# Performance work log

Measured on AMD Instinct MI355X. Metric: run time of the kernel, lower is better.

Reference implementation:

```python
import jax, jax.numpy as jnp
import numpy as np

EPS = 1e-05
KERNEL_SIZE = 9
KERNEL_VOL = float(KERNEL_SIZE ** 3)

_DN = ("NDHWC", "DHWIO", "NDHWC")


def _box_sum(x, k=KERNEL_SIZE):
    """Sliding-window sum over a k^3 box with SAME zero padding.

    The TF module uses a dense all-ones (k,k,k) conv3d; an all-ones kernel is
    separable, so three 1D passes compute the identical result with O(k) work.
    x: (B, D1, D2, D3, 1) float.
    """
    for kshape in ((k, 1, 1), (1, k, 1), (1, 1, k)):
        w = jnp.ones(kshape + (1, 1), dtype=x.dtype)
        x = jax.lax.conv_general_dilated(
            x, w, window_strides=(1, 1, 1), padding="SAME",
            dimension_numbers=_DN)
    return x


def setup_inputs() -> dict:
    key = jax.random.key(0)
    k1, k2 = jax.random.split(key)
    shape = (2, 192, 192, 192)
    y_true = jax.random.uniform(k1, shape, dtype=jnp.float32)
    y_pred = jax.random.uniform(k2, shape, dtype=jnp.float32)
    return {"y_true": y_true, "y_pred": y_pred}


def reference(y_true, y_pred):
    # Expand (B, D1, D2, D3) -> (B, D1, D2, D3, 1) as in the TF call().
    if y_true.ndim == 4:
        y_true = y_true[..., None]
        y_pred = y_pred[..., None]

    t_sum = _box_sum(y_true)
    p_sum = _box_sum(y_pred)
    tp_sum = _box_sum(y_true * y_pred)

    t_avg = t_sum / KERNEL_VOL
    p_avg = p_sum / KERNEL_VOL

    cross = tp_sum - p_avg * t_sum
    num = cross * cross + EPS  # the DEBUG1 variant returns `num` directly
    return num
```

## Files before the change

### kernel.cpp

```cpp
#include <hip/hip_runtime.h>


#define N 192
#define RSTRIDE 46

#define LDS_BARRIER() asm volatile("s_waitcnt lgkmcnt(0)\n\ts_barrier" ::: "memory")

__global__ __launch_bounds__(1024, 4)
void lncc_kernel(const float* __restrict__ t_in,
                 const float* __restrict__ p_in,
                 float* __restrict__ out)
{
    __shared__ __align__(16) float rowT[3 * 32 * RSTRIDE];
    __shared__ float pcol[3 * 32 * 32];

    const int bid = blockIdx.x;
    int xy, Z, z0;
    if (bid < 64) {
        xy = bid >> 3;
        Z  = 24;
        z0 = (bid & 7) * 24;
    } else {
        const int q  = bid - 64;
        xy = 8 + q / 7;
        const int zi = q % 7;
        if (zi < 3) { Z = 28; z0 = zi * 28; }
        else        { Z = 27; z0 = 84 + (zi - 3) * 27; }
    }
    const int b  = xy / 36;
    const int t6 = xy % 36;
    const int y0 = (t6 / 6) * 32, x0 = (t6 % 6) * 32;
    const int tid = threadIdx.x;

    const int  lf   = tid / 320;
    const int  ls   = tid - lf * 320;
    const int  lry  = ls >> 3;
    const int  lxq  = ls & 7;
    const int  lgy  = y0 - 4 + lry;
    const int  lgx0 = x0 - 4 + 4 * lxq;
    const bool lactive = (tid < 960);
    const bool lyok = ((unsigned)lgy < (unsigned)N);

    const int  cf  = tid >> 8;
    const int  cyq = (tid >> 5) & 7;
    const int  cx  = tid & 31;
    const bool cactive = (tid < 768);

    const int gx = tid & 31;
    const int gy = tid >> 5;

    const size_t plane = (size_t)N * N;
    const float* tb = t_in + (size_t)b * N * plane;
    const float* pb = p_in + (size_t)b * N * plane;
    float*       ob = out  + (size_t)b * N * plane
                           + (size_t)(y0 + gy) * N + (x0 + gx);

    const int lgyc = lyok ? lgy : 0;
    const float* const trow = tb + (size_t)lgyc * N;
    const float* const prow = pb + (size_t)lgyc * N;
    const float* const arow = (lf == 1) ? prow : trow;

    float ring_t[9], ring_p[9], ring_tp[9];
    float sum_t = 0.f, sum_p = 0.f, sum_tp = 0.f;
    #pragma unroll
    for (int i = 0; i < 9; ++i) { ring_t[i] = 0.f; ring_p[i] = 0.f; ring_tp[i] = 0.f; }

    const float4 z4 = make_float4(0.f, 0.f, 0.f, 0.f);

    {
        const int zp0 = z0 - 4;
        float4 fa0 = z4, fa1 = z4, fa2 = z4, fc0 = z4, fc1 = z4, fc2 = z4;
        if (((unsigned)zp0 < (unsigned)N) && lactive && lyok) {
            const float* ar = arow + (size_t)zp0 * plane;
            const float* cr = prow + (size_t)zp0 * plane;
            const int g0 = lgx0, g1 = lgx0 + 4, g2 = lgx0 + 8;
            if ((unsigned)g0 < (unsigned)N) {
                fa0 = *(const float4*)(ar + g0);
                if (lf == 2) fc0 = *(const float4*)(cr + g0);
            }
            if ((unsigned)g1 < (unsigned)N) {
                fa1 = *(const float4*)(ar + g1);
                if (lf == 2) fc1 = *(const float4*)(cr + g1);
            }
            if ((unsigned)g2 < (unsigned)N) {
                fa2 = *(const float4*)(ar + g2);
                if (lf == 2) fc2 = *(const float4*)(cr + g2);
            }
        }
        if (lactive) {
            float4 A0 = fa0, A1 = fa1, A2 = fa2;
            if (lf == 2) {
                A0.x *= fc0.x; A0.y *= fc0.y; A0.z *= fc0.z; A0.w *= fc0.w;
                A1.x *= fc1.x; A1.y *= fc1.y; A1.z *= fc1.z; A1.w *= fc1.w;
                A2.x *= fc2.x; A2.y *= fc2.y; A2.z *= fc2.z; A2.w *= fc2.w;
            }
            const float v0 = A0.x, v1 = A0.y, v2  = A0.z, v3  = A0.w;
            const float v4 = A1.x, v5 = A1.y, v6  = A1.z, v7  = A1.w;
            const float v8 = A2.x, v9 = A2.y, v10 = A2.z, v11 = A2.w;
            float s0 = ((v0+v1) + (v2+v3)) + ((v4+v5) + (v6+v7)) + v8;
            float s1 = s0 - v0 + v9;
            float s2 = s1 - v1 + v10;
            float s3 = s2 - v2 + v11;
            float* wp = &rowT[(lf * 32 + 4 * lxq) * RSTRIDE + lry];
            wp[0]           = s0;
            wp[RSTRIDE]     = s1;
            wp[2 * RSTRIDE] = s2;
            wp[3 * RSTRIDE] = s3;
        }
    }

    #pragma unroll 1
    for (int k = 0; k < 4; ++k) {
      #pragma unroll
      for (int r = 0; r < 9; ++r) {
        const int i  = k * 9 + r;
        const int zp = z0 - 4 + i;
        const int zn = zp + 1;
        const bool vi = (i < Z + 8)     && ((unsigned)zp < (unsigned)N);
        const bool vn = (i + 1 < Z + 8) && ((unsigned)zn < (unsigned)N);

        float4 fa0 = z4, fa1 = z4, fa2 = z4, fc0 = z4, fc1 = z4, fc2 = z4;
        if (vn && lactive && lyok) {
            const float* ar = arow + (size_t)zn * plane;
            const float* cr = prow + (size_t)zn * plane;
            const int g0 = lgx0, g1 = lgx0 + 4, g2 = lgx0 + 8;
            if ((unsigned)g0 < (unsigned)N) {
                fa0 = *(const float4*)(ar + g0);
                if (lf == 2) fc0 = *(const float4*)(cr + g0);
            }
            if ((unsigned)g1 < (unsigned)N) {
                fa1 = *(const float4*)(ar + g1);
                if (lf == 2) fc1 = *(const float4*)(cr + g1);
            }
            if ((unsigned)g2 < (unsigned)N) {
                fa2 = *(const float4*)(ar + g2);
                if (lf == 2) fc2 = *(const float4*)(cr + g2);
            }
        }
        LDS_BARRIER();

        if (vi && cactive) {
            const float* rb = &rowT[(cf * 32 + cx) * RSTRIDE + 4 * cyq];
            const float2 u0 = *(const float2*)(rb + 0);
            const float2 u1 = *(const float2*)(rb + 2);
            const float2 u2 = *(const float2*)(rb + 4);
            const float2 u3 = *(const float2*)(rb + 6);
            const float2 u4 = *(const float2*)(rb + 8);
            const float2 u5 = *(const float2*)(rb + 10);
            const float w0=u0.x, w1=u0.y, w2=u1.x,  w3=u1.y;
            const float w4=u2.x, w5=u2.y, w6=u3.x,  w7=u3.y;
            const float w8=u4.x, w9=u4.y, w10=u5.x, w11=u5.y;
            float c0 = ((w0+w1)+(w2+w3)) + ((w4+w5)+(w6+w7)) + w8;
            float c1 = c0 - w0 + w9;
            float c2 = c1 - w1 + w10;
            float c3 = c2 - w2 + w11;
            float* pc = &pcol[cf * 1024 + (4 * cyq) * 32 + cx];
            pc[0]  = c0;
            pc[32] = c1;
            pc[64] = c2;
            pc[96] = c3;
        }
        LDS_BARRIER();

        float Pt = 0.f, Pp = 0.f, Ptp = 0.f;
        if (vi) {
            Pt  = pcol[       gy * 32 + gx];
            Pp  = pcol[1024 + gy * 32 + gx];
            Ptp = pcol[2048 + gy * 32 + gx];
        }
        sum_t  += Pt  - ring_t[r];  ring_t[r]  = Pt;
        sum_p  += Pp  - ring_p[r];  ring_p[r]  = Pp;
        sum_tp += Ptp - ring_tp[r]; ring_tp[r] = Ptp;
        if (i >= 8 && i < Z + 8) {
            const float cross = sum_tp - (sum_p * (1.0f / 729.0f)) * sum_t;
            ob[(size_t)(z0 + i - 8) * plane] = cross * cross + 1e-5f;
        }

        if (vn && lactive) {
            float4 A0 = fa0, A1 = fa1, A2 = fa2;
            if (lf == 2) {
                A0.x *= fc0.x; A0.y *= fc0.y; A0.z *= fc0.z; A0.w *= fc0.w;
                A1.x *= fc1.x; A1.y *= fc1.y; A1.z *= fc1.z; A1.w *= fc1.w;
                A2.x *= fc2.x; A2.y *= fc2.y; A2.z *= fc2.z; A2.w *= fc2.w;
            }
            const float v0 = A0.x, v1 = A0.y, v2  = A0.z, v3  = A0.w;
            const float v4 = A1.x, v5 = A1.y, v6  = A1.z, v7  = A1.w;
            const float v8 = A2.x, v9 = A2.y, v10 = A2.z, v11 = A2.w;
            float s0 = ((v0+v1) + (v2+v3)) + ((v4+v5) + (v6+v7)) + v8;
            float s1 = s0 - v0 + v9;
            float s2 = s1 - v1 + v10;
            float s3 = s2 - v2 + v11;
            float* wp = &rowT[(lf * 32 + 4 * lxq) * RSTRIDE + lry];
            wp[0]           = s0;
            wp[RSTRIDE]     = s1;
            wp[2 * RSTRIDE] = s2;
            wp[3 * RSTRIDE] = s3;
        }
      }
    }
}

extern "C" void kernel_launch(void* const* d_in, const int* in_sizes, int n_in,
                              void* d_out, int out_size, void* d_ws, size_t ws_size,
                              hipStream_t stream) {
    const float* y_true = (const float*)d_in[0];
    const float* y_pred = (const float*)d_in[1];
    float* out = (float*)d_out;
    dim3 grid(512);
    dim3 block(1024);
    hipLaunchKernelGGL(lncc_kernel, grid, block, 0, stream, y_true, y_pred, out);
}
```

Before: 223.7 us.

## Double-buffer row sums and fuse column pass to drop a barrier per slice

Removes the separate column-sum stage and its pcol buffer. Each output thread now reads 9 transposed row-sum values per field directly from LDS, and the row-sum buffer is double-buffered so only one barrier per z-slice is needed instead of two. The row-sum computation is deferred to the next iteration, using values held in registers. The cost is more LDS reads per thread (27 scalar loads instead of 3) and a larger LDS footprint (about 35 KB instead of about 30 KB), which may reduce occupancy.

```diff
diff --git a/kernel.cpp b/kernel.cpp
--- a/kernel.cpp
+++ b/kernel.cpp
@@ -3,6 +3,8 @@
 
 #define N 192
 #define RSTRIDE 46
+#define RBUF (3 * 32 * RSTRIDE)
+#define FSTRIDE (32 * RSTRIDE)
 
 #define LDS_BARRIER() asm volatile("s_waitcnt lgkmcnt(0)\n\ts_barrier" ::: "memory")
 
@@ -11,8 +13,7 @@
                  const float* __restrict__ p_in,
                  float* __restrict__ out)
 {
-    __shared__ __align__(16) float rowT[3 * 32 * RSTRIDE];
-    __shared__ float pcol[3 * 32 * 32];
+    __shared__ __align__(16) float rowT[2 * RBUF];
 
     const int bid = blockIdx.x;
     int xy, Z, z0;
@@ -41,11 +42,6 @@
     const bool lactive = (tid < 960);
     const bool lyok = ((unsigned)lgy < (unsigned)N);
 
-    const int  cf  = tid >> 8;
-    const int  cyq = (tid >> 5) & 7;
-    const int  cx  = tid & 31;
-    const bool cactive = (tid < 768);
-
     const int gx = tid & 31;
     const int gy = tid >> 5;
 
@@ -60,12 +56,16 @@
     const float* const prow = pb + (size_t)lgyc * N;
     const float* const arow = (lf == 1) ? prow : trow;
 
+    float* const       wpA   = &rowT[(lf * 32 + 4 * lxq) * RSTRIDE + lry];
+    const float* const ybase = &rowT[gx * RSTRIDE + gy];
+
     float ring_t[9], ring_p[9], ring_tp[9];
     float sum_t = 0.f, sum_p = 0.f, sum_tp = 0.f;
     #pragma unroll
     for (int i = 0; i < 9; ++i) { ring_t[i] = 0.f; ring_p[i] = 0.f; ring_tp[i] = 0.f; }
 
     const float4 z4 = make_float4(0.f, 0.f, 0.f, 0.f);
+    float4 cur0 = z4, cur1 = z4, cur2 = z4;
 
     {
         const int zp0 = z0 - 4;
@@ -94,18 +94,7 @@
                 A1.x *= fc1.x; A1.y *= fc1.y; A1.z *= fc1.z; A1.w *= fc1.w;
                 A2.x *= fc2.x; A2.y *= fc2.y; A2.z *= fc2.z; A2.w *= fc2.w;
             }
-            const float v0 = A0.x, v1 = A0.y, v2  = A0.z, v3  = A0.w;
-            const float v4 = A1.x, v5 = A1.y, v6  = A1.z, v7  = A1.w;
-            const float v8 = A2.x, v9 = A2.y, v10 = A2.z, v11 = A2.w;
-            float s0 = ((v0+v1) + (v2+v3)) + ((v4+v5) + (v6+v7)) + v8;
-            float s1 = s0 - v0 + v9;
-            float s2 = s1 - v1 + v10;
-            float s3 = s2 - v2 + v11;
-            float* wp = &rowT[(lf * 32 + 4 * lxq) * RSTRIDE + lry];
-            wp[0]           = s0;
-            wp[RSTRIDE]     = s1;
-            wp[2 * RSTRIDE] = s2;
-            wp[3 * RSTRIDE] = s3;
+            cur0 = A0; cur1 = A1; cur2 = A2;
         }
     }
 
@@ -116,8 +105,8 @@
         const int i  = k * 9 + r;
         const int zp = z0 - 4 + i;
         const int zn = zp + 1;
-        const bool vi = (i < Z + 8)     && ((unsigned)zp < (unsigned)N);
         const bool vn = (i + 1 < Z + 8) && ((unsigned)zn < (unsigned)N);
+        const int rofs = ((k + r) & 1) * RBUF;
 
         float4 fa0 = z4, fa1 = z4, fa2 = z4, fc0 = z4, fc1 = z4, fc2 = z4;
         if (vn && lactive && lyok) {
@@ -137,64 +126,50 @@
                 if (lf == 2) fc2 = *(const float4*)(cr + g2);
             }
         }
-        LDS_BARRIER();
 
-        if (vi && cactive) {
-            const float* rb = &rowT[(cf * 32 + cx) * RSTRIDE + 4 * cyq];
-            const float2 u0 = *(const float2*)(rb + 0);
-            const float2 u1 = *(const float2*)(rb + 2);
-            const float2 u2 = *(const float2*)(rb + 4);
-            const float2 u3 = *(const float2*)(rb + 6);
-            const float2 u4 = *(const float2*)(rb + 8);
-            const float2 u5 = *(const float2*)(rb + 10);
-            const float w0=u0.x, w1=u0.y, w2=u1.x,  w3=u1.y;
-            const float w4=u2.x, w5=u2.y, w6=u3.x,  w7=u3.y;
-            const float w8=u4.x, w9=u4.y, w10=u5.x, w11=u5.y;
-            float c0 = ((w0+w1)+(w2+w3)) + ((w4+w5)+(w6+w7)) + w8;
-            float c1 = c0 - w0 + w9;
-            float c2 = c1 - w1 + w10;
-            float c3 = c2 - w2 + w11;
-            float* pc = &pcol[cf * 1024 + (4 * cyq) * 32 + cx];
-            pc[0]  = c0;
-            pc[32] = c1;
-            pc[64] = c2;
-            pc[96] = c3;
+        if (lactive) {
+            const float v0 = cur0.x, v1 = cur0.y, v2  = cur0.z, v3  = cur0.w;
+            const float v4 = cur1.x, v5 = cur1.y, v6  = cur1.z, v7  = cur1.w;
+            const float v8 = cur2.x, v9 = cur2.y, v10 = cur2.z, v11 = cur2.w;
+            float s0 = ((v0+v1) + (v2+v3)) + ((v4+v5) + (v6+v7)) + v8;
+            float s1 = s0 - v0 + v9;
+            float s2 = s1 - v1 + v10;
+            float s3 = s2 - v2 + v11;
+            float* wp = wpA + rofs;
+            wp[0]           = s0;
+            wp[RSTRIDE]     = s1;
+            wp[2 * RSTRIDE] = s2;
+            wp[3 * RSTRIDE] = s3;
         }
         LDS_BARRIER();
 
-        float Pt = 0.f, Pp = 0.f, Ptp = 0.f;
-        if (vi) {
-            Pt  = pcol[       gy * 32 + gx];
-            Pp  = pcol[1024 + gy * 32 + gx];
-            Ptp = pcol[2048 + gy * 32 + gx];
+        {
+            const float* a = ybase + rofs;
+            const float Pt  = ((a[0]+a[1]) + (a[2]+a[3]))
+                            + ((a[4]+a[5]) + (a[6]+a[7])) + a[8];
+            const float* p2 = a + FSTRIDE;
+            const float Pp  = ((p2[0]+p2[1]) + (p2[2]+p2[3]))
+                            + ((p2[4]+p2[5]) + (p2[6]+p2[7])) + p2[8];
+            const float* q2 = a + 2 * FSTRIDE;
+            const float Ptp = ((q2[0]+q2[1]) + (q2[2]+q2[3]))
+                            + ((q2[4]+q2[5]) + (q2[6]+q2[7])) + q2[8];
+            sum_t  += Pt  - ring_t[r];  ring_t[r]  = Pt;
+            sum_p  += Pp  - ring_p[r];  ring_p[r]  = Pp;
+            sum_tp += Ptp - ring_tp[r]; ring_tp[r] = Ptp;
         }
-        sum_t  += Pt  - ring_t[r];  ring_t[r]  = Pt;
-        sum_p  += Pp  - ring_p[r];  ring_p[r]  = Pp;
-        sum_tp += Ptp - ring_tp[r]; ring_tp[r] = Ptp;
         if (i >= 8 && i < Z + 8) {
             const float cross = sum_tp - (sum_p * (1.0f / 729.0f)) * sum_t;
             ob[(size_t)(z0 + i - 8) * plane] = cross * cross + 1e-5f;
         }
 
-        if (vn && lactive) {
+        if (lactive) {
             float4 A0 = fa0, A1 = fa1, A2 = fa2;
             if (lf == 2) {
                 A0.x *= fc0.x; A0.y *= fc0.y; A0.z *= fc0.z; A0.w *= fc0.w;
                 A1.x *= fc1.x; A1.y *= fc1.y; A1.z *= fc1.z; A1.w *= fc1.w;
                 A2.x *= fc2.x; A2.y *= fc2.y; A2.z *= fc2.z; A2.w *= fc2.w;
             }
-            const float v0 = A0.x, v1 = A0.y, v2  = A0.z, v3  = A0.w;
-            const float v4 = A1.x, v5 = A1.y, v6  = A1.z, v7  = A1.w;
-            const float v8 = A2.x, v9 = A2.y, v10 = A2.z, v11 = A2.w;
-            float s0 = ((v0+v1) + (v2+v3)) + ((v4+v5) + (v6+v7)) + v8;
-            float s1 = s0 - v0 + v9;
-            float s2 = s1 - v1 + v10;
-            float s3 = s2 - v2 + v11;
-            float* wp = &rowT[(lf * 32 + 4 * lxq) * RSTRIDE + lry];
-            wp[0]           = s0;
-            wp[RSTRIDE]     = s1;
-            wp[2 * RSTRIDE] = s2;
-            wp[3 * RSTRIDE] = s3;
+            cur0 = A0; cur1 = A1; cur2 = A2;
         }
       }
     }
```

After: 241.3 us. 1.08x slower.
